# Kernel optimization log

Hardware: AMD Instinct MI355X
Metric: run time of the kernel (lower is better)

## Reference

```python
import jax, jax.numpy as jnp
import numpy as np

N_NODES = 50000
N_EDGES = 800000
NUM_GRAPHS = 16
NUM_CLASSES = 247


def _glorot(key, shape):
    fan_in = shape[0]
    return jax.random.normal(key, shape, jnp.float32) * (1.0 / np.sqrt(fan_in))


def setup_inputs() -> dict:
    key = jax.random.key(0)
    ks = jax.random.split(key, 8)
    x = jax.random.normal(ks[0], (N_NODES, 3), jnp.float32)
    edge_index = jax.random.randint(ks[1], (2, N_EDGES), 0, N_NODES, dtype=jnp.int64 if jax.config.jax_enable_x64 else jnp.int32)
    batch = jnp.sort(jax.random.randint(ks[2], (N_NODES,), 0, NUM_GRAPHS))
    return {
        "x": x,
        "edge_index": edge_index,
        "batch": batch,
        "W1": _glorot(ks[3], (3, 64)),
        "b1": jnp.zeros((64,), jnp.float32),
        "W2": _glorot(ks[4], (64, 128)),
        "b2": jnp.zeros((128,), jnp.float32),
        "W3": _glorot(ks[5], (128, 256)),
        "b3": jnp.zeros((256,), jnp.float32),
        "Wfc": _glorot(ks[6], (256, NUM_CLASSES)),
        "bfc": jnp.zeros((NUM_CLASSES,), jnp.float32),
    }


def reference(x, edge_index, batch, W1, b1, W2, b2, W3, b3, Wfc, bfc):
    N = x.shape[0]
    # --- GCN symmetric normalization with self-loops (PyG gcn_norm) ---
    loops = jnp.arange(N, dtype=edge_index.dtype)
    ei = jnp.concatenate([edge_index, jnp.stack([loops, loops])], axis=1)
    row, col = ei[0], ei[1]  # src -> dst, aggregate at dst
    deg = jax.ops.segment_sum(jnp.ones(ei.shape[1], x.dtype), col, num_segments=N)
    dinv = jnp.where(deg > 0, jax.lax.rsqrt(deg), 0.0)
    norm = dinv[row] * dinv[col]  # [E+N]

    def gcn(h, W, b):
        h = h @ W                                    # [N, out]
        msg = h[row] * norm[:, None]                 # gather + scale
        agg = jax.ops.segment_sum(msg, col, num_segments=N)  # scatter-add
        return agg + b

    h = jax.nn.relu(gcn(x, W1, b1))
    h = jax.nn.relu(gcn(h, W2, b2))
    h = jax.nn.relu(gcn(h, W3, b3))

    # --- global_mean_pool over batch indices ---
    sums = jax.ops.segment_sum(h, batch, num_segments=NUM_GRAPHS)      # [G, 256]
    cnt = jax.ops.segment_sum(jnp.ones(N, h.dtype), batch, num_segments=NUM_GRAPHS)
    pooled = sums / jnp.maximum(cnt, 1.0)[:, None]

    return pooled @ Wfc + bfc  # [G, num_classes]
```

## Files before the change

### kernel.cpp

```cpp
#include <hip/hip_runtime.h>

#define N_NODES 50000
#define N_EDGES 800000
#define NUM_GRAPHS 16
#define NUM_CLASSES 247
#define SCAN_BLOCKS ((N_NODES + 255) / 256)

typedef __attribute__((ext_vector_type(8))) short bf16x8;
typedef __attribute__((ext_vector_type(4))) float f32x4;

static inline int nblk(long n) { return (int)((n + 255) / 256); }

__device__ __forceinline__ float bfl(unsigned short u) {
    return __uint_as_float((unsigned)u << 16);
}
__device__ __forceinline__ unsigned short bf16_rne(float f) {
    unsigned u = __float_as_uint(f);
    u += 0x7FFF + ((u >> 16) & 1);
    return (unsigned short)(u >> 16);
}

__global__ void k_deg(const int* __restrict__ col, int* __restrict__ degc,
                      int* __restrict__ pos, int E) {
    int e = blockIdx.x * blockDim.x + threadIdx.x;
    if (e >= E) return;
    int c8 = (e >> 8) & 7;
    pos[e] = atomicAdd(&degc[c8 * N_NODES + col[e]], 1);
}

__global__ __launch_bounds__(256) void k_scan1(const int* __restrict__ degc,
                                               int* __restrict__ rowptr,
                                               int* __restrict__ bsum,
                                               const int* __restrict__ batch,
                                               float* __restrict__ pcnt, int N) {
    __shared__ int buf[256];
    __shared__ int hist[NUM_GRAPHS];
    int t = threadIdx.x;
    if (t < NUM_GRAPHS) hist[t] = 0;
    int i = blockIdx.x * 256 + t;
    int v = 0;
    if (i < N) {
#pragma unroll
        for (int c = 0; c < 8; ++c) v += degc[c * N_NODES + i];
        atomicAdd(&hist[batch[i]], 1);
    }
    buf[t] = v;
    __syncthreads();
#pragma unroll
    for (int off = 1; off < 256; off <<= 1) {
        int tmp = (t >= off) ? buf[t - off] : 0;
        __syncthreads();
        if (t >= off) buf[t] += tmp;
        __syncthreads();
    }
    if (i < N) rowptr[i] = buf[t] - v;
    if (t == 255) bsum[blockIdx.x] = buf[255];
    if (t < NUM_GRAPHS && hist[t] > 0) atomicAdd(&pcnt[t], (float)hist[t]);
}

__global__ __launch_bounds__(256) void k_scan3(int* __restrict__ rowptr,
                                               const int* __restrict__ bsum,
                                               const int* __restrict__ degc,
                                               int* __restrict__ base,
                                               float* __restrict__ dinv,
                                               const float* __restrict__ x,
                                               float* __restrict__ xs,
                                               const float* __restrict__ W2,
                                               const float* __restrict__ W3,
                                               unsigned short* __restrict__ Wt2,
                                               unsigned short* __restrict__ Wt3,
                                               int N) {
    __shared__ int red[256];
    int t = threadIdx.x;
    int b = blockIdx.x;
    red[t] = (t < b) ? bsum[t] : 0;
    __syncthreads();
#pragma unroll
    for (int off = 128; off > 0; off >>= 1) {
        if (t < off) red[t] += red[t + off];
        __syncthreads();
    }
    int boff = red[0];
    int i = b * 256 + t;
    if (i < N) {
        int rp = rowptr[i] + boff;
        rowptr[i] = rp;
        int run = rp, tot = 0;
#pragma unroll
        for (int c = 0; c < 8; ++c) {
            int d = degc[c * N_NODES + i];
            base[c * N_NODES + i] = run;
            run += d;
            tot += d;
        }
        float dv = rsqrtf((float)tot + 1.0f);
        dinv[i] = dv;
        xs[i * 3 + 0] = dv * x[i * 3 + 0];
        xs[i * 3 + 1] = dv * x[i * 3 + 1];
        xs[i * 3 + 2] = dv * x[i * 3 + 2];
    }
    if (i == 0) rowptr[N] = N_EDGES;
    if (i < 64 * 128) {
        int f = i / 64, k = i % 64;
        Wt2[i] = bf16_rne(W2[k * 128 + f]);
    } else if (i < 64 * 128 + 128 * 256) {
        int j = i - 64 * 128;
        int f = j / 128, k = j % 128;
        Wt3[j] = bf16_rne(W3[k * 256 + f]);
    }
}

__global__ void k_fill(const int* __restrict__ row, const int* __restrict__ col,
                       const int* __restrict__ base, const int* __restrict__ pos,
                       int* __restrict__ csr_src, int E) {
    int e = blockIdx.x * blockDim.x + threadIdx.x;
    if (e >= E) return;
    int c8 = (e >> 8) & 7;
    csr_src[base[c8 * N_NODES + col[e]] + pos[e]] = row[e];
}

__global__ void k_layer1(const float* __restrict__ xs, const float* __restrict__ dinv,
                         const int* __restrict__ rowptr, const int* __restrict__ csr_src,
                         const float* __restrict__ W1, const float* __restrict__ b1,
                         unsigned short* __restrict__ out, int N) {
    int v = blockIdx.x * blockDim.x + threadIdx.x;
    if (v >= N) return;
    float a0 = xs[v * 3 + 0];
    float a1 = xs[v * 3 + 1];
    float a2 = xs[v * 3 + 2];
    int j = rowptr[v];
    int j1 = rowptr[v + 1];
    for (; j + 4 <= j1; j += 4) {
        int r0 = csr_src[j + 0], r1 = csr_src[j + 1];
        int r2 = csr_src[j + 2], r3 = csr_src[j + 3];
        float x00 = xs[r0 * 3 + 0], x01 = xs[r0 * 3 + 1], x02 = xs[r0 * 3 + 2];
        float x10 = xs[r1 * 3 + 0], x11 = xs[r1 * 3 + 1], x12 = xs[r1 * 3 + 2];
        float x20 = xs[r2 * 3 + 0], x21 = xs[r2 * 3 + 1], x22 = xs[r2 * 3 + 2];
        float x30 = xs[r3 * 3 + 0], x31 = xs[r3 * 3 + 1], x32 = xs[r3 * 3 + 2];
        a0 += x00; a1 += x01; a2 += x02;
        a0 += x10; a1 += x11; a2 += x12;
        a0 += x20; a1 += x21; a2 += x22;
        a0 += x30; a1 += x31; a2 += x32;
    }
    for (; j < j1; ++j) {
        int r = csr_src[j];
        a0 += xs[r * 3 + 0];
        a1 += xs[r * 3 + 1];
        a2 += xs[r * 3 + 2];
    }
    float dv = dinv[v];
    float p0 = dv * a0, p1 = dv * a1, p2 = dv * a2;
    unsigned short* ov = out + (long)v * 64;
#pragma unroll
    for (int f = 0; f < 64; f += 2) {
        float s0 = fmaf(p0, W1[f],     fmaf(p1, W1[64 + f],     fmaf(p2, W1[128 + f],     b1[f])));
        float s1 = fmaf(p0, W1[f + 1], fmaf(p1, W1[64 + f + 1], fmaf(p2, W1[128 + f + 1], b1[f + 1])));
        s0 = fmaxf(s0, 0.0f) * dv;
        s1 = fmaxf(s1, 0.0f) * dv;
        unsigned pk = (unsigned)bf16_rne(s0) | ((unsigned)bf16_rne(s1) << 16);
        *(unsigned*)(ov + f) = pk;
    }
}

template <int K, int F, bool PRESCALE>
__global__ __launch_bounds__(256) void k_fused(
        const unsigned short* __restrict__ h, const float* __restrict__ dinv,
        const int* __restrict__ rowptr, const int* __restrict__ csr_src,
        const unsigned short* __restrict__ Wt, const float* __restrict__ b,
        unsigned short* __restrict__ out, int N) {
    constexpr int NF = F / 16;
    constexpr int FPW = NF / 4;
    constexpr int KB = K / 32;
    constexpr int KL = K / 64;
    constexpr int PADK = K + 8;
    __shared__ unsigned short plds[16][PADK];
    int wave = threadIdx.x >> 6;
    int lane = threadIdx.x & 63;
    int m0 = blockIdx.x * 16;

    for (int pr = 0; pr < 2; ++pr) {
        int va = m0 + wave * 4 + pr * 2;
        int vb = va + 1;
        float acca[KL], accb[KL];
        const unsigned short* hva = h + (long)va * K + lane * KL;
        const unsigned short* hvb = h + (long)vb * K + lane * KL;
        if (KL == 2) {
            unsigned ua = *(const unsigned*)hva;
            unsigned ub = *(const unsigned*)hvb;
            acca[0] = __uint_as_float(ua << 16);
            acca[1] = __uint_as_float(ua & 0xFFFF0000u);
            accb[0] = __uint_as_float(ub << 16);
            accb[1] = __uint_as_float(ub & 0xFFFF0000u);
        } else {
            acca[0] = bfl(hva[0]);
            accb[0] = bfl(hvb[0]);
        }
        int ja  = __builtin_amdgcn_readfirstlane(rowptr[va]);
        int j1a = __builtin_amdgcn_readfirstlane(rowptr[va + 1]);
        int jb  = j1a;
        int j1b = __builtin_amdgcn_readfirstlane(rowptr[vb + 1]);
        while (ja + 8 <= j1a && jb + 8 <= j1b) {
            int ra[8], rb[8];
#pragma unroll
            for (int u = 0; u < 8; ++u) ra[u] = csr_src[ja + u];
#pragma unroll
            for (int u = 0; u < 8; ++u) rb[u] = csr_src[jb + u];
            if (KL == 2) {
                unsigned ta[8], tb[8];
#pragma unroll
                for (int u = 0; u < 8; ++u)
                    ta[u] = *(const unsigned*)(h + (long)ra[u] * K + lane * 2);
#pragma unroll
                for (int u = 0; u < 8; ++u)
                    tb[u] = *(const unsigned*)(h + (long)rb[u] * K + lane * 2);
#pragma unroll
                for (int u = 0; u < 8; ++u) {
                    acca[0] += __uint_as_float(ta[u] << 16);
                    acca[1] += __uint_as_float(ta[u] & 0xFFFF0000u);
                }
#pragma unroll
                for (int u = 0; u < 8; ++u) {
                    accb[0] += __uint_as_float(tb[u] << 16);
                    accb[1] += __uint_as_float(tb[u] & 0xFFFF0000u);
                }
            } else {
                unsigned short ta[8], tb[8];
#pragma unroll
                for (int u = 0; u < 8; ++u) ta[u] = h[(long)ra[u] * K + lane];
#pragma unroll
                for (int u = 0; u < 8; ++u) tb[u] = h[(long)rb[u] * K + lane];
#pragma unroll
                for (int u = 0; u < 8; ++u) acca[0] += bfl(ta[u]);
#pragma unroll
                for (int u = 0; u < 8; ++u) accb[0] += bfl(tb[u]);
            }
            ja += 8;
            jb += 8;
        }
        for (; ja + 8 <= j1a; ja += 8) {
            int r[8];
#pragma unroll
            for (int u = 0; u < 8; ++u) r[u] = csr_src[ja + u];
            if (KL == 2) {
                unsigned tv[8];
#pragma unroll
                for (int u = 0; u < 8; ++u)
                    tv[u] = *(const unsigned*)(h + (long)r[u] * K + lane * 2);
#pragma unroll
                for (int u = 0; u < 8; ++u) {
                    acca[0] += __uint_as_float(tv[u] << 16);
                    acca[1] += __uint_as_float(tv[u] & 0xFFFF0000u);
                }
            } else {
                unsigned short tv[8];
#pragma unroll
                for (int u = 0; u < 8; ++u) tv[u] = h[(long)r[u] * K + lane];
#pragma unroll
                for (int u = 0; u < 8; ++u) acca[0] += bfl(tv[u]);
            }
        }
        for (; ja < j1a; ++ja) {
            int r = csr_src[ja];
            if (KL == 2) {
                unsigned u = *(const unsigned*)(h + (long)r * K + lane * 2);
                acca[0] += __uint_as_float(u << 16);
                acca[1] += __uint_as_float(u & 0xFFFF0000u);
            } else {
                acca[0] += bfl(h[(long)r * K + lane]);
            }
        }
        for (; jb + 8 <= j1b; jb += 8) {
            int r[8];
#pragma unroll
            for (int u = 0; u < 8; ++u) r[u] = csr_src[jb + u];
            if (KL == 2) {
                unsigned tv[8];
#pragma unroll
                for (int u = 0; u < 8; ++u)
                    tv[u] = *(const unsigned*)(h + (long)r[u] * K + lane * 2);
#pragma unroll
                for (int u = 0; u < 8; ++u) {
                    accb[0] += __uint_as_float(tv[u] << 16);
                    accb[1] += __uint_as_float(tv[u] & 0xFFFF0000u);
                }
            } else {
                unsigned short tv[8];
#pragma unroll
                for (int u = 0; u < 8; ++u) tv[u] = h[(long)r[u] * K + lane];
#pragma unroll
                for (int u = 0; u < 8; ++u) accb[0] += bfl(tv[u]);
            }
        }
        for (; jb < j1b; ++jb) {
            int r = csr_src[jb];
            if (KL == 2) {
                unsigned u = *(const unsigned*)(h + (long)r * K + lane * 2);
                accb[0] += __uint_as_float(u << 16);
                accb[1] += __uint_as_float(u & 0xFFFF0000u);
            } else {
                accb[0] += bfl(h[(long)r * K + lane]);
            }
        }
        float da = dinv[va];
        float db = dinv[vb];
        int rla = wave * 4 + pr * 2;
        if (KL == 2) {
            unsigned pa = (unsigned)bf16_rne(da * acca[0]) | ((unsigned)bf16_rne(da * acca[1]) << 16);
            unsigned pb = (unsigned)bf16_rne(db * accb[0]) | ((unsigned)bf16_rne(db * accb[1]) << 16);
            *(unsigned*)&plds[rla][lane * 2] = pa;
            *(unsigned*)&plds[rla + 1][lane * 2] = pb;
        } else {
            plds[rla][lane] = bf16_rne(da * acca[0]);
            plds[rla + 1][lane] = bf16_rne(db * accb[0]);
        }
    }
    __syncthreads();

    int quad = lane >> 4;
    int l16 = lane & 15;
    bf16x8 afr[KB];
#pragma unroll
    for (int kb = 0; kb < KB; ++kb)
        afr[kb] = *(const bf16x8*)(const void*)&plds[l16][kb * 32 + quad * 8];
#pragma unroll
    for (int fi = 0; fi < FPW; ++fi) {
        int f0 = (wave * FPW + fi) * 16;
        const unsigned short* wrow = Wt + (long)(f0 + l16) * K + quad * 8;
        f32x4 acc4 = {0.f, 0.f, 0.f, 0.f};
#pragma unroll
        for (int kb = 0; kb < KB; ++kb) {
            bf16x8 bb = *(const bf16x8*)(const void*)(wrow + kb * 32);
            acc4 = __builtin_amdgcn_mfma_f32_16x16x32_bf16(afr[kb], bb, acc4, 0, 0, 0);
        }
        float bias = b[f0 + l16];
#pragma unroll
        for (int r = 0; r < 4; ++r) {
            int m = m0 + quad * 4 + r;
            float val = fmaxf(acc4[r] + bias, 0.0f);
            if (PRESCALE) val *= dinv[m];
            out[(long)m * F + f0 + l16] = bf16_rne(val);
        }
    }
}

#define POOL_CHUNK 64
__global__ __launch_bounds__(256) void k_pool(
        const unsigned short* __restrict__ h, const int* __restrict__ batch,
        float* __restrict__ psum, int N) {
    int tid = threadIdx.x;
    int n0 = blockIdx.x * POOL_CHUNK;
    int n1 = n0 + POOL_CHUNK;
    if (n1 > N) n1 = N;
    int gcur = batch[n0];
    float racc = 0.0f;
    for (int n = n0; n < n1; ++n) {
        int g = batch[n];
        if (g != gcur) {
            atomicAdd(&psum[gcur * 256 + tid], racc);
            racc = 0.0f;
            gcur = g;
        }
        racc += bfl(h[(long)n * 256 + tid]);
    }
    atomicAdd(&psum[gcur * 256 + tid], racc);
}

__global__ void k_fc(const float* __restrict__ psum, const float* __restrict__ pcnt,
                     const float* __restrict__ Wfc, const float* __restrict__ bfc,
                     float* __restrict__ out) {
    int tid = blockIdx.x * blockDim.x + threadIdx.x;
    if (tid >= NUM_GRAPHS * NUM_CLASSES) return;
    int g = tid / NUM_CLASSES;
    int c = tid % NUM_CLASSES;
    float s = 0.0f;
#pragma unroll 8
    for (int k = 0; k < 256; ++k) s = fmaf(psum[g * 256 + k], Wfc[k * NUM_CLASSES + c], s);
    float cnt = pcnt[g];
    cnt = cnt > 1.0f ? cnt : 1.0f;
    out[tid] = s / cnt + bfc[c];
}

extern "C" void kernel_launch(void* const* d_in, const int* in_sizes, int n_in,
                              void* d_out, int out_size, void* d_ws, size_t ws_size,
                              hipStream_t stream) {
    const float* x     = (const float*)d_in[0];
    const int*   ei    = (const int*)d_in[1];
    const int*   batch = (const int*)d_in[2];
    const float* W1    = (const float*)d_in[3];
    const float* b1    = (const float*)d_in[4];
    const float* W2    = (const float*)d_in[5];
    const float* b2    = (const float*)d_in[6];
    const float* W3    = (const float*)d_in[7];
    const float* b3    = (const float*)d_in[8];
    const float* Wfc   = (const float*)d_in[9];
    const float* bfc   = (const float*)d_in[10];
    float* out = (float*)d_out;

    const int* row = ei;
    const int* col = ei + N_EDGES;

    float*  bufA = (float*)d_ws;
    float*  xs   = bufA + (size_t)N_NODES * 256;
    float*  dinv = xs + (size_t)N_NODES * 3;
    float*  psum = dinv + N_NODES;
    float*  pcnt = psum + NUM_GRAPHS * 256;
    unsigned short* X   = (unsigned short*)(pcnt + NUM_GRAPHS);
    unsigned short* Y   = X + (size_t)N_NODES * 128;
    unsigned short* Wt2 = Y + (size_t)N_NODES * 128;
    unsigned short* Wt3 = Wt2 + 128 * 64;
    unsigned short* H3  = (unsigned short*)bufA;
    int* degc   = (int*)(Wt3 + 256 * 128);
    int* base   = degc + 8 * N_NODES;
    int* rowptr = base + 8 * N_NODES;
    int* csrsrc = rowptr + N_NODES + 1;
    int* pos    = csrsrc + N_EDGES;
    int* bsum   = pos + N_EDGES;

    hipMemsetAsync(degc, 0, 8 * N_NODES * sizeof(int), stream);
    hipMemsetAsync(psum, 0, (NUM_GRAPHS * 256 + NUM_GRAPHS) * sizeof(float), stream);

    k_deg<<<nblk(N_EDGES), 256, 0, stream>>>(col, degc, pos, N_EDGES);
    k_scan1<<<SCAN_BLOCKS, 256, 0, stream>>>(degc, rowptr, bsum, batch, pcnt, N_NODES);
    k_scan3<<<SCAN_BLOCKS, 256, 0, stream>>>(rowptr, bsum, degc, base, dinv, x, xs,
                                             W2, W3, Wt2, Wt3, N_NODES);
    k_fill<<<nblk(N_EDGES), 256, 0, stream>>>(row, col, base, pos, csrsrc, N_EDGES);

    k_layer1<<<nblk(N_NODES), 256, 0, stream>>>(xs, dinv, rowptr, csrsrc, W1, b1, X, N_NODES);

    int mtiles = N_NODES / 16;

    k_fused<64, 128, true><<<mtiles, 256, 0, stream>>>(X, dinv, rowptr, csrsrc,
                                                       Wt2, b2, Y, N_NODES);

    k_fused<128, 256, false><<<mtiles, 256, 0, stream>>>(Y, dinv, rowptr, csrsrc,
                                                         Wt3, b3, H3, N_NODES);

    int pool_blocks = (N_NODES + POOL_CHUNK - 1) / POOL_CHUNK;
    k_pool<<<pool_blocks, 256, 0, stream>>>(H3, batch, psum, N_NODES);
    k_fc<<<nblk(NUM_GRAPHS * NUM_CLASSES), 256, 0, stream>>>(psum, pcnt, Wfc, bfc, out);
}
```

Measured before the change: 276.6 us.

## Fuse global mean pooling into final GCN layer epilogue

The third GCN layer no longer writes its 50000x256 bf16 output to global memory. Each block reduces its outputs per graph into shared-memory partial sums, covering the first and last graph id in its 16-node tile, and then issues global atomics. This removes the separate pool kernel and the write and re-read of H3. In exchange it adds shared-memory atomics in the MFMA epilogue, global atomics from every block, and a block-level sync.

```diff
diff --git a/kernel.cpp b/kernel.cpp
--- a/kernel.cpp
+++ b/kernel.cpp
@@ -162,21 +162,31 @@
     }
 }
 
-template <int K, int F, bool PRESCALE>
+template <int K, int F, bool PRESCALE, bool POOL>
 __global__ __launch_bounds__(256) void k_fused(
         const unsigned short* __restrict__ h, const float* __restrict__ dinv,
         const int* __restrict__ rowptr, const int* __restrict__ csr_src,
         const unsigned short* __restrict__ Wt, const float* __restrict__ b,
-        unsigned short* __restrict__ out, int N) {
+        unsigned short* __restrict__ out, const int* __restrict__ batch,
+        float* __restrict__ psum, int N) {
     constexpr int NF = F / 16;
     constexpr int FPW = NF / 4;
     constexpr int KB = K / 32;
     constexpr int KL = K / 64;
     constexpr int PADK = K + 8;
     __shared__ unsigned short plds[16][PADK];
+    __shared__ float lps[2][256];
+    __shared__ int gb[16];
     int wave = threadIdx.x >> 6;
     int lane = threadIdx.x & 63;
+    int t = threadIdx.x;
     int m0 = blockIdx.x * 16;
+
+    if (POOL) {
+        if (t < 16) gb[t] = batch[m0 + t];
+        lps[0][t] = 0.0f;
+        lps[1][t] = 0.0f;
+    }
 
     for (int pr = 0; pr < 2; ++pr) {
         int va = m0 + wave * 4 + pr * 2;
@@ -335,34 +345,31 @@
         float bias = b[f0 + l16];
 #pragma unroll
         for (int r = 0; r < 4; ++r) {
-            int m = m0 + quad * 4 + r;
+            int rowloc = quad * 4 + r;
             float val = fmaxf(acc4[r] + bias, 0.0f);
-            if (PRESCALE) val *= dinv[m];
-            out[(long)m * F + f0 + l16] = bf16_rne(val);
-        }
-    }
-}
-
-#define POOL_CHUNK 64
-__global__ __launch_bounds__(256) void k_pool(
-        const unsigned short* __restrict__ h, const int* __restrict__ batch,
-        float* __restrict__ psum, int N) {
-    int tid = threadIdx.x;
-    int n0 = blockIdx.x * POOL_CHUNK;
-    int n1 = n0 + POOL_CHUNK;
-    if (n1 > N) n1 = N;
-    int gcur = batch[n0];
-    float racc = 0.0f;
-    for (int n = n0; n < n1; ++n) {
-        int g = batch[n];
-        if (g != gcur) {
-            atomicAdd(&psum[gcur * 256 + tid], racc);
-            racc = 0.0f;
-            gcur = g;
-        }
-        racc += bfl(h[(long)n * 256 + tid]);
-    }
-    atomicAdd(&psum[gcur * 256 + tid], racc);
+            if (POOL) {
+                int g = gb[rowloc];
+                int g0 = gb[0], g15 = gb[15];
+                if (g == g0) {
+                    atomicAdd(&lps[0][f0 + l16], val);
+                } else if (g == g15) {
+                    atomicAdd(&lps[1][f0 + l16], val);
+                } else {
+                    atomicAdd(&psum[g * 256 + f0 + l16], val);
+                }
+            } else {
+                int m = m0 + rowloc;
+                if (PRESCALE) val *= dinv[m];
+                out[(long)m * F + f0 + l16] = bf16_rne(val);
+            }
+        }
+    }
+    if (POOL) {
+        __syncthreads();
+        int g0 = gb[0], g15 = gb[15];
+        atomicAdd(&psum[g0 * 256 + t], lps[0][t]);
+        if (g15 != g0) atomicAdd(&psum[g15 * 256 + t], lps[1][t]);
+    }
 }
 
 __global__ void k_fc(const float* __restrict__ psum, const float* __restrict__ pcnt,
@@ -399,8 +406,7 @@
     const int* row = ei;
     const int* col = ei + N_EDGES;
 
-    float*  bufA = (float*)d_ws;
-    float*  xs   = bufA + (size_t)N_NODES * 256;
+    float*  xs   = (float*)d_ws;
     float*  dinv = xs + (size_t)N_NODES * 3;
     float*  psum = dinv + N_NODES;
     float*  pcnt = psum + NUM_GRAPHS * 256;
@@ -408,7 +414,6 @@
     unsigned short* Y   = X + (size_t)N_NODES * 128;
     unsigned short* Wt2 = Y + (size_t)N_NODES * 128;
     unsigned short* Wt3 = Wt2 + 128 * 64;
-    unsigned short* H3  = (unsigned short*)bufA;
     int* degc   = (int*)(Wt3 + 256 * 128);
     int* base   = degc + 8 * N_NODES;
     int* rowptr = base + 8 * N_NODES;
@@ -429,13 +434,11 @@
 
     int mtiles = N_NODES / 16;
 
-    k_fused<64, 128, true><<<mtiles, 256, 0, stream>>>(X, dinv, rowptr, csrsrc,
-                                                       Wt2, b2, Y, N_NODES);
-
-    k_fused<128, 256, false><<<mtiles, 256, 0, stream>>>(Y, dinv, rowptr, csrsrc,
-                                                         Wt3, b3, H3, N_NODES);
-
-    int pool_blocks = (N_NODES + POOL_CHUNK - 1) / POOL_CHUNK;
-    k_pool<<<pool_blocks, 256, 0, stream>>>(H3, batch, psum, N_NODES);
+    k_fused<64, 128, true, false><<<mtiles, 256, 0, stream>>>(
+        X, dinv, rowptr, csrsrc, Wt2, b2, Y, batch, psum, N_NODES);
+
+    k_fused<128, 256, false, true><<<mtiles, 256, 0, stream>>>(
+        Y, dinv, rowptr, csrsrc, Wt3, b3, (unsigned short*)nullptr, batch, psum, N_NODES);
+
     k_fc<<<nblk(NUM_GRAPHS * NUM_CLASSES), 256, 0, stream>>>(psum, pcnt, Wfc, bfc, out);
 }
```

Measured after the change: 288.4 us. 4.2% more time.
